# Kernel tuning notes

Hardware: AMD Instinct MI355X
Metric: run time of the kernel (lower is better)

Reference implementation:

```python
import jax, jax.numpy as jnp
import numpy as np

N = 20000   # nodes
E = 256000  # edges
G = 64      # graphs
EPS = 1e-5  # batchnorm eps


def setup_inputs() -> dict:
    key = jax.random.key(0)
    ks = jax.random.split(key, 20)
    inp = {}
    inp['x'] = jax.random.normal(ks[0], (N, 6), dtype=jnp.float32)
    inp['edge_index'] = jax.random.randint(ks[1], (2, E), 0, N)
    inp['batch'] = jnp.sort(jax.random.randint(ks[2], (N,), 0, G))
    conv_dims = [(6, 32), (32, 64), (64, 128), (128, 1024)]
    ki = 3
    for li, (a, b) in enumerate(conv_dims, 1):
        inp[f'W{li}'] = jax.random.normal(ks[ki], (a, b), dtype=jnp.float32) / np.sqrt(a).astype(np.float32); ki += 1
        inp[f'b{li}'] = jnp.zeros((b,), jnp.float32)
        inp[f'g{li}'] = jnp.ones((b,), jnp.float32)
        inp[f'be{li}'] = jnp.zeros((b,), jnp.float32)
    fc_dims = [(1024, 512), (512, 256), (256, 64)]
    for li, (a, b) in enumerate(fc_dims, 5):
        inp[f'W{li}'] = jax.random.normal(ks[ki], (a, b), dtype=jnp.float32) / np.sqrt(a).astype(np.float32); ki += 1
        inp[f'b{li}'] = jnp.zeros((b,), jnp.float32)
        if li < 7:
            inp[f'g{li}'] = jnp.ones((b,), jnp.float32)
            inp[f'be{li}'] = jnp.zeros((b,), jnp.float32)
    return inp


def _bn(h, g, be):
    # training-mode BatchNorm1d: biased variance over dim 0
    m = h.mean(axis=0)
    v = h.var(axis=0)
    return g * (h - m) * jax.lax.rsqrt(v + EPS) + be


def reference(x, edge_index, batch,
              W1, b1, g1, be1, W2, b2, g2, be2,
              W3, b3, g3, be3, W4, b4, g4, be4,
              W5, b5, g5, be5, W6, b6, g6, be6,
              W7, b7):
    loops = jnp.arange(N)
    src = jnp.concatenate([edge_index[0], loops])  # [E+N], message sources
    dst = jnp.concatenate([edge_index[1], loops])  # [E+N], aggregation targets
    deg = jax.ops.segment_sum(jnp.ones(E + N, x.dtype), dst, num_segments=N)
    dinv = jax.lax.rsqrt(deg)                      # deg >= 1 (self-loops)
    norm = dinv[src] * dinv[dst]                   # symmetric GCN normalization

    def gcn(h, W, b):
        h = h @ W                                   # [N, out]
        agg = jax.ops.segment_sum(norm[:, None] * h[src], dst, num_segments=N)
        return agg + b

    h = jax.nn.relu(_bn(gcn(x, W1, b1), g1, be1))
    h = jax.nn.relu(_bn(gcn(h, W2, b2), g2, be2))
    h = jax.nn.relu(_bn(gcn(h, W3, b3), g3, be3))
    h = jax.nn.relu(_bn(gcn(h, W4, b4), g4, be4))
    p = jax.ops.segment_max(h, batch, num_segments=G)  # global max pool [G, 1024]
    p = jax.nn.relu(_bn(p @ W5 + b5, g5, be5))
    p = jax.nn.relu(_bn(p @ W6 + b6, g6, be6))
    y = p @ W7 + b7
    n = jnp.maximum(jnp.linalg.norm(y, axis=1, keepdims=True), 1e-12)
    return y / n
```

## Files before the change

### kernel.cpp

```cpp
#include <hip/hip_runtime.h>
#include <math.h>

#define NN 20000
#define EE 256000
#define GG 64
#define CDIV(a,b) (((a)+(b)-1)/(b))
#define RB4 157

typedef __attribute__((ext_vector_type(8))) short bf16x8;
typedef __attribute__((ext_vector_type(4))) float f32x4;

__device__ __forceinline__ unsigned fkey(float f) {
  unsigned u = __float_as_uint(f);
  return (u & 0x80000000u) ? ~u : (u | 0x80000000u);
}
__device__ __forceinline__ float fdec(unsigned k) {
  unsigned u = (k & 0x80000000u) ? (k ^ 0x80000000u) : ~k;
  return __uint_as_float(u);
}
__device__ __forceinline__ unsigned short rne_bf16(float f) {
  unsigned u = __float_as_uint(f);
  unsigned r = (u + 0x7fffu + ((u >> 16) & 1u)) >> 16;
  return (unsigned short)r;
}


__global__ void k_prep(int* deg) {
  int i = blockIdx.x*blockDim.x + threadIdx.x;
  if (i < NN) deg[i] = 1;
}

__global__ void k_deg(const int* __restrict__ dst, int* deg) {
  int i = blockIdx.x*blockDim.x + threadIdx.x;
  if (i < EE) atomicAdd(&deg[dst[i]], 1);
}

__global__ __launch_bounds__(256) void k_scan_bsum(const int* __restrict__ deg,
                                                   int* __restrict__ bsum) {
  __shared__ int red[256];
  int b = blockIdx.x, t = threadIdx.x;
  int idx = b*1024 + t*4;
  int4 v = make_int4(0,0,0,0);
  if (idx < NN) v = *(const int4*)&deg[idx];
  red[t] = v.x + v.y + v.z + v.w;
  __syncthreads();
  for (int off = 128; off > 0; off >>= 1) {
    if (t < off) red[t] += red[t+off];
    __syncthreads();
  }
  if (t == 0) bsum[b] = red[0];
}

__global__ __launch_bounds__(256) void k_scan_apply(
    const int* __restrict__ deg, const int* __restrict__ bsum,
    int* __restrict__ offsets, int* __restrict__ cursor, float* __restrict__ dinv) {
  __shared__ int base_s;
  __shared__ int tsum[256];
  int b = blockIdx.x, t = threadIdx.x;
  if (t == 0) {
    int s = 0;
    for (int i = 0; i < b; ++i) s += bsum[i];
    base_s = s;
  }
  int idx = b*1024 + t*4;
  int4 v = make_int4(0,0,0,0);
  if (idx < NN) v = *(const int4*)&deg[idx];
  tsum[t] = v.x + v.y + v.z + v.w;
  __syncthreads();
  for (int off = 1; off < 256; off <<= 1) {
    int u = (t >= off) ? tsum[t-off] : 0;
    __syncthreads();
    tsum[t] += u;
    __syncthreads();
  }
  int excl = (t == 0) ? 0 : tsum[t-1];
  if (idx < NN) {
    int base = base_s + excl;
    int o0 = base;
    int o1 = o0 + v.x;
    int o2 = o1 + v.y;
    int o3 = o2 + v.z;
    *(int4*)&offsets[idx] = make_int4(o0,o1,o2,o3);
    *(int4*)&cursor[idx]  = make_int4(o0,o1,o2,o3);
    float4 dv;
    dv.x = rsqrtf((float)v.x); dv.y = rsqrtf((float)v.y);
    dv.z = rsqrtf((float)v.z); dv.w = rsqrtf((float)v.w);
    *(float4*)&dinv[idx] = dv;
    if (idx + 4 == NN) offsets[NN] = o3 + v.w;
  }
}

__global__ void k_fill(const int* __restrict__ srcv, const int* __restrict__ dstv,
                       const float* __restrict__ dinv, int* cursor,
                       int* __restrict__ csr_src, float* __restrict__ csr_w) {
  int i = blockIdx.x*blockDim.x + threadIdx.x;
  if (i < EE) {
    int s = srcv[i], d = dstv[i];
    int pos = atomicAdd(&cursor[d], 1);
    csr_src[pos] = s;
    csr_w[pos] = dinv[s] * dinv[d];
  } else if (i < EE + NN) {
    int n = i - EE;
    int pos = atomicAdd(&cursor[n], 1);
    csr_src[pos] = n;
    float di = dinv[n];
    csr_w[pos] = di * di;
  }
}


template<int C, int TX, int TY>
__global__ void k_agg(const float* __restrict__ in, const int* __restrict__ offsets,
                      const int* __restrict__ csr_src, const float* __restrict__ csr_w,
                      float* __restrict__ out) {
  int node = blockIdx.x * TY + threadIdx.y;
  if (node >= NN) return;
  int x = threadIdx.x;
  int k0 = offsets[node], k1 = offsets[node+1];
  if (x < C) {
    float acc = 0.f;
    for (int k = k0; k < k1; ++k) {
      int s = csr_src[k];
      float w = csr_w[k];
      acc += w * in[s*C + x];
    }
    out[node*C + x] = acc;
  }
}

template<int C, int TY>
__global__ void k_agg_f4(const float* __restrict__ in, const float* __restrict__ st,
                         const float* __restrict__ g, const float* __restrict__ be,
                         const int* __restrict__ offsets, const int* __restrict__ csr_src,
                         const float* __restrict__ csr_w, float* __restrict__ out) {
  int node = blockIdx.x*TY + threadIdx.y;
  if (node >= NN) return;
  int c0 = threadIdx.x*4;
  float4 mean = *(const float4*)&st[c0];
  float4 rstd = *(const float4*)&st[C+c0];
  float4 gv = *(const float4*)&g[c0];
  float4 bv = *(const float4*)&be[c0];
  float sx = gv.x*rstd.x, hx = bv.x - mean.x*sx;
  float sy = gv.y*rstd.y, hy = bv.y - mean.y*sy;
  float sz = gv.z*rstd.z, hz = bv.z - mean.z*sz;
  float sw = gv.w*rstd.w, hw = bv.w - mean.w*sw;
  int k0 = offsets[node], k1 = offsets[node+1];
  float a0=0.f,a1=0.f,a2=0.f,a3=0.f;
  for (int k = k0; k < k1; ++k) {
    int s = csr_src[k]; float w = csr_w[k];
    float4 v = *(const float4*)&in[s*C + c0];
    a0 += w*fmaxf(v.x*sx+hx, 0.f);
    a1 += w*fmaxf(v.y*sy+hy, 0.f);
    a2 += w*fmaxf(v.z*sz+hz, 0.f);
    a3 += w*fmaxf(v.w*sw+hw, 0.f);
  }
  *(float4*)&out[node*C+c0] = make_float4(a0,a1,a2,a3);
}

__global__ void k_agg_bf_f4(const float* __restrict__ in, const float* __restrict__ st,
                            const float* __restrict__ g, const float* __restrict__ be,
                            const int* __restrict__ offsets, const int* __restrict__ csr_src,
                            const float* __restrict__ csr_w, unsigned short* __restrict__ out) {
  int node = blockIdx.x*8 + threadIdx.y;
  if (node >= NN) return;
  int c0 = threadIdx.x*4;
  float4 mean = *(const float4*)&st[c0];
  float4 rstd = *(const float4*)&st[128+c0];
  float4 gv = *(const float4*)&g[c0];
  float4 bv = *(const float4*)&be[c0];
  float sx = gv.x*rstd.x, hx = bv.x - mean.x*sx;
  float sy = gv.y*rstd.y, hy = bv.y - mean.y*sy;
  float sz = gv.z*rstd.z, hz = bv.z - mean.z*sz;
  float sw = gv.w*rstd.w, hw = bv.w - mean.w*sw;
  int k0 = offsets[node], k1 = offsets[node+1];
  float a0=0.f,a1=0.f,a2=0.f,a3=0.f;
  for (int k = k0; k < k1; ++k) {
    int s = csr_src[k]; float w = csr_w[k];
    float4 v = *(const float4*)&in[s*128 + c0];
    a0 += w*fmaxf(v.x*sx+hx, 0.f);
    a1 += w*fmaxf(v.y*sy+hy, 0.f);
    a2 += w*fmaxf(v.z*sz+hz, 0.f);
    a3 += w*fmaxf(v.w*sw+hw, 0.f);
  }
  ushort4 o;
  o.x = rne_bf16(a0); o.y = rne_bf16(a1); o.z = rne_bf16(a2); o.w = rne_bf16(a3);
  *(ushort4*)&out[node*128 + c0] = o;
}

__global__ void k_wprep(const float* __restrict__ W, unsigned short* __restrict__ out) {
  int i = blockIdx.x*256 + threadIdx.x;
  if (i >= 128*1024) return;
  int k = i >> 10, c = i & 1023;
  out[c*128 + k] = rne_bf16(W[i]);
}


template<int K, int OUT, int ROWS>
__global__ __launch_bounds__(256) void k_gemm_small(
    const float* __restrict__ A, const float* __restrict__ W,
    float* __restrict__ out, float* __restrict__ pstats) {
  constexpr int RG  = 256 / OUT;
  constexpr int RPT = ROWS / RG;
  __shared__ float Ws[K*OUT];
  __shared__ float As[ROWS*K];
  __shared__ float reds[2][RG][OUT];
  int t = threadIdx.x;
  for (int i = t; i < K*OUT; i += 256) Ws[i] = W[i];
  int row0 = blockIdx.x * ROWS;
  for (int i = t; i < ROWS*K; i += 256) As[i] = A[row0*K + i];
  __syncthreads();
  int j  = t % OUT;
  int rg = t / OUT;
  float acc[RPT] = {};
  for (int k = 0; k < K; ++k) {
    float w = Ws[k*OUT + j];
    #pragma unroll
    for (int i = 0; i < RPT; ++i)
      acc[i] += As[(rg*RPT + i)*K + k] * w;
  }
  float s = 0.f, ss = 0.f;
  #pragma unroll
  for (int i = 0; i < RPT; ++i) {
    out[(row0 + rg*RPT + i)*OUT + j] = acc[i];
    s += acc[i]; ss += acc[i]*acc[i];
  }
  reds[0][rg][j] = s; reds[1][rg][j] = ss;
  __syncthreads();
  if (rg == 0) {
    float S = 0.f, SS = 0.f;
    #pragma unroll
    for (int r = 0; r < RG; ++r) { S += reds[0][r][j]; SS += reds[1][r][j]; }
    int p = blockIdx.x & 15;
    atomicAdd(&pstats[p*2*OUT + j], S);
    atomicAdd(&pstats[p*2*OUT + OUT + j], SS);
  }
}

template<int C>
__global__ void k_finalize_ps(const float* __restrict__ pstats, float* __restrict__ stats) {
  int c = blockIdx.x*64 + threadIdx.x;
  if (c >= C) return;
  float s = 0.f, ss = 0.f;
  #pragma unroll
  for (int p = 0; p < 16; ++p) { s += pstats[p*2*C + c]; ss += pstats[p*2*C + C + c]; }
  float m = s * (1.f/NN);
  float v = ss * (1.f/NN) - m*m;
  stats[c] = m;
  stats[C+c] = rsqrtf(v + 1e-5f);
}


__global__ __launch_bounds__(256) void k_gemm_l4_mfma(
    const unsigned short* __restrict__ A, const unsigned short* __restrict__ Bt,
    const int* __restrict__ batch,
    float* __restrict__ ps4, unsigned* __restrict__ pmax, unsigned* __restrict__ pmin) {
  __shared__ unsigned short As[128*128];
  __shared__ unsigned short Bs[128*128];
  int t = threadIdx.x;
  int row0 = blockIdx.x * 128;
  int col0 = blockIdx.y * 128;
  #pragma unroll
  for (int j = 0; j < 8; ++j) {
    int c = j*256 + t;
    int r = c >> 4, ck = c & 15;
    int rg = row0 + r;
    ulonglong2 v; v.x = 0; v.y = 0;
    if (rg < NN) v = *(const ulonglong2*)&A[rg*128 + ck*8];
    *(ulonglong2*)&As[r*128 + (ck ^ (r & 7))*8] = v;
  }
  #pragma unroll
  for (int j = 0; j < 8; ++j) {
    int c = j*256 + t;
    int r = c >> 4, ck = c & 15;
    ulonglong2 v = *(const ulonglong2*)&Bt[(col0 + r)*128 + ck*8];
    *(ulonglong2*)&Bs[r*128 + (ck ^ (r & 7))*8] = v;
  }
  __syncthreads();

  int w = t >> 6, l = t & 63;
  int wr = w >> 1, wc = w & 1;
  int lrow = l & 15, lk = l >> 4;
  f32x4 acc[4][4] = {};
  #pragma unroll
  for (int ks = 0; ks < 4; ++ks) {
    int kc = ks*4 + lk;
    bf16x8 a[4], b[4];
    #pragma unroll
    for (int m = 0; m < 4; ++m) {
      int r = wr*64 + m*16 + lrow;
      a[m] = *(const bf16x8*)&As[r*128 + (kc ^ (r & 7))*8];
    }
    #pragma unroll
    for (int n = 0; n < 4; ++n) {
      int r = wc*64 + n*16 + lrow;
      b[n] = *(const bf16x8*)&Bs[r*128 + (kc ^ (r & 7))*8];
    }
    #pragma unroll
    for (int m = 0; m < 4; ++m)
      #pragma unroll
      for (int n = 0; n < 4; ++n)
        acc[m][n] = __builtin_amdgcn_mfma_f32_16x16x32_bf16(a[m], b[n], acc[m][n], 0, 0, 0);
  }

  int rbase = row0 + wr*64;
  float s[4] = {}, ss[4] = {};
  float mx[4], mn[4];
  #pragma unroll
  for (int n = 0; n < 4; ++n) { mx[n] = -3.4e38f; mn[n] = 3.4e38f; }
  #pragma unroll
  for (int m = 0; m < 4; ++m)
    #pragma unroll
    for (int r = 0; r < 4; ++r) {
      int row_g = rbase + m*16 + lk*4 + r;
      if (row_g < NN) {
        #pragma unroll
        for (int n = 0; n < 4; ++n) {
          float v = acc[m][n][r];
          s[n] += v; ss[n] += v*v;
          mx[n] = fmaxf(mx[n], v); mn[n] = fminf(mn[n], v);
        }
      }
    }
  #pragma unroll
  for (int n = 0; n < 4; ++n) {
    s[n]  += __shfl_xor(s[n], 16);  s[n]  += __shfl_xor(s[n], 32);
    ss[n] += __shfl_xor(ss[n], 16); ss[n] += __shfl_xor(ss[n], 32);
  }

  int rlast_b = min(row0 + 127, NN - 1);
  int glo_b = batch[row0], ghi_b = batch[rlast_b];
  bool block_same = (glo_b == ghi_b);
  if (block_same) {
    #pragma unroll
    for (int n = 0; n < 4; ++n) {
      mx[n] = fmaxf(mx[n], __shfl_xor(mx[n], 16)); mx[n] = fmaxf(mx[n], __shfl_xor(mx[n], 32));
      mn[n] = fminf(mn[n], __shfl_xor(mn[n], 16)); mn[n] = fminf(mn[n], __shfl_xor(mn[n], 32));
    }
  }

  __syncthreads();
  float* scr_s = (float*)As;
  float* scr_p = (float*)Bs;
  if (l < 16) {
    #pragma unroll
    for (int n = 0; n < 4; ++n) {
      int si = (((wr*2 + wc)*4 + n)*16 + l)*2;
      scr_s[si]   = s[n];
      scr_s[si+1] = ss[n];
      if (block_same) { scr_p[si] = mx[n]; scr_p[si+1] = mn[n]; }
    }
  }
  __syncthreads();
  if (wr == 0 && l < 16) {
    #pragma unroll
    for (int n = 0; n < 4; ++n) {
      int si0 = (((0*2 + wc)*4 + n)*16 + l)*2;
      int si1 = (((1*2 + wc)*4 + n)*16 + l)*2;
      int cg  = col0 + wc*64 + n*16 + l;
      ps4[(size_t)blockIdx.x*2048 + cg]        = scr_s[si0]   + scr_s[si1];
      ps4[(size_t)blockIdx.x*2048 + 1024 + cg] = scr_s[si0+1] + scr_s[si1+1];
      if (block_same) {
        float bmx = fmaxf(scr_p[si0],   scr_p[si1]);
        float bmn = fminf(scr_p[si0+1], scr_p[si1+1]);
        if (bmx > -3.0e38f) atomicMax(&pmax[glo_b*1024 + cg], fkey(bmx));
        if (bmn <  3.0e38f) atomicMin(&pmin[glo_b*1024 + cg], fkey(bmn));
      }
    }
  }
  if (!block_same && rbase < NN) {
    int rlast = min(rbase + 63, NN - 1);
    int glo = batch[rbase], ghi = batch[rlast];
    if (glo == ghi) {
      #pragma unroll
      for (int n = 0; n < 4; ++n) {
        mx[n] = fmaxf(mx[n], __shfl_xor(mx[n], 16)); mx[n] = fmaxf(mx[n], __shfl_xor(mx[n], 32));
        mn[n] = fminf(mn[n], __shfl_xor(mn[n], 16)); mn[n] = fminf(mn[n], __shfl_xor(mn[n], 32));
      }
      if (l < 16) {
        #pragma unroll
        for (int n = 0; n < 4; ++n) {
          int cg = col0 + wc*64 + n*16 + l;
          atomicMax(&pmax[glo*1024 + cg], fkey(mx[n]));
          atomicMin(&pmin[glo*1024 + cg], fkey(mn[n]));
        }
      }
    } else {
      int gb[4][4];
      #pragma unroll
      for (int m = 0; m < 4; ++m)
        #pragma unroll
        for (int r = 0; r < 4; ++r) {
          int row_g = rbase + m*16 + lk*4 + r;
          gb[m][r] = (row_g < NN) ? batch[row_g] : -1;
        }
      for (int g = glo; g <= ghi; ++g) {
        float gmx[4], gmn[4];
        #pragma unroll
        for (int n = 0; n < 4; ++n) { gmx[n] = -3.4e38f; gmn[n] = 3.4e38f; }
        #pragma unroll
        for (int m = 0; m < 4; ++m)
          #pragma unroll
          for (int r = 0; r < 4; ++r) {
            bool in_g = (gb[m][r] == g);
            #pragma unroll
            for (int n = 0; n < 4; ++n) {
              float v = acc[m][n][r];
              gmx[n] = in_g ? fmaxf(gmx[n], v) : gmx[n];
              gmn[n] = in_g ? fminf(gmn[n], v) : gmn[n];
            }
          }
        #pragma unroll
        for (int n = 0; n < 4; ++n) {
          gmx[n] = fmaxf(gmx[n], __shfl_xor(gmx[n], 16)); gmx[n] = fmaxf(gmx[n], __shfl_xor(gmx[n], 32));
          gmn[n] = fminf(gmn[n], __shfl_xor(gmn[n], 16)); gmn[n] = fminf(gmn[n], __shfl_xor(gmn[n], 32));
        }
        if (l < 16) {
          #pragma unroll
          for (int n = 0; n < 4; ++n) {
            int cg = col0 + wc*64 + n*16 + l;
            if (gmx[n] > -3.0e38f) atomicMax(&pmax[g*1024 + cg], fkey(gmx[n]));
            if (gmn[n] <  3.0e38f) atomicMin(&pmin[g*1024 + cg], fkey(gmn[n]));
          }
        }
      }
    }
  }
}

__global__ void k_finalize_l4(const float* __restrict__ ps4, float* __restrict__ stats) {
  int c = blockIdx.x*256 + threadIdx.x;
  float s = 0.f, ss = 0.f;
  #pragma unroll 8
  for (int rb = 0; rb < RB4; ++rb) {
    s  += ps4[(size_t)rb*2048 + c];
    ss += ps4[(size_t)rb*2048 + 1024 + c];
  }
  float m = s * (1.f/NN);
  float v = ss * (1.f/NN) - m*m;
  stats[c] = m;
  stats[1024 + c] = rsqrtf(v + 1e-5f);
}

__global__ void k_bnpool(const unsigned* __restrict__ pmax, const unsigned* __restrict__ pmin,
                         const float* __restrict__ stats, const float* __restrict__ g,
                         const float* __restrict__ be, float* __restrict__ p) {
  int i = blockIdx.x*256 + threadIdx.x;
  if (i >= 64*1024) return;
  int c = i & 1023;
  float mean = stats[c], rstd = stats[1024+c];
  float sc = g[c]*rstd, sh = be[c] - mean*sc;
  float v = (sc >= 0.f) ? fdec(pmax[i]) : fdec(pmin[i]);
  p[i] = fmaxf(v*sc + sh, 0.f);
}


template<int K, int OUT, int KT>
__global__ __launch_bounds__(256) void k_fc_tile(
    const float* __restrict__ A, const float* __restrict__ W,
    float* __restrict__ out) {
  __shared__ float As[64][KT];
  __shared__ float Ws[KT][64];
  int t = threadIdx.y*64 + threadIdx.x;
  int j0 = blockIdx.x*64;
  int k0 = blockIdx.y*KT;
  #pragma unroll 4
  for (int i = t; i < 64*KT/4; i += 256) {
    int r  = i / (KT/4);
    int c4 = i % (KT/4);
    float4 v = *(const float4*)&A[r*K + k0 + c4*4];
    *(float4*)&As[r][c4*4] = v;
  }
  #pragma unroll 4
  for (int i = t; i < KT*16; i += 256) {
    int k  = i / 16;
    int c4 = i % 16;
    float4 v = *(const float4*)&W[(k0+k)*OUT + j0 + c4*4];
    *(float4*)&Ws[k][c4*4] = v;
  }
  __syncthreads();
  int j  = threadIdx.x;
  int r0 = threadIdx.y*16;
  float acc[16] = {};
  for (int kk = 0; kk < KT; ++kk) {
    float w = Ws[kk][j];
    #pragma unroll
    for (int i = 0; i < 16; ++i) acc[i] += As[r0+i][kk] * w;
  }
  #pragma unroll
  for (int i = 0; i < 16; ++i) atomicAdd(&out[(r0+i)*OUT + j0 + j], acc[i]);
}

__global__ __launch_bounds__(512) void k_bn_rows(
    float* __restrict__ h, const float* __restrict__ g,
    const float* __restrict__ be, int C) {
  int c = blockIdx.x*64 + threadIdx.x;
  int y = threadIdx.y;
  float v[8];
  float s = 0.f, ss = 0.f;
  #pragma unroll
  for (int i = 0; i < 8; ++i) {
    v[i] = h[(y*8+i)*C + c];
    s += v[i]; ss += v[i]*v[i];
  }
  __shared__ float rs[8][64], rss[8][64], bc[2][64];
  rs[y][threadIdx.x] = s; rss[y][threadIdx.x] = ss;
  __syncthreads();
  if (y == 0) {
    s = 0.f; ss = 0.f;
    #pragma unroll
    for (int i = 0; i < 8; ++i) { s += rs[i][threadIdx.x]; ss += rss[i][threadIdx.x]; }
    float m = s*(1.f/64.f);
    float var = ss*(1.f/64.f) - m*m;
    float rstd = rsqrtf(var + 1e-5f);
    float sc = g[c]*rstd;
    bc[0][threadIdx.x] = sc;
    bc[1][threadIdx.x] = be[c] - m*sc;
  }
  __syncthreads();
  float sc = bc[0][threadIdx.x], sh = bc[1][threadIdx.x];
  #pragma unroll
  for (int i = 0; i < 8; ++i)
    h[(y*8+i)*C + c] = fmaxf(v[i]*sc + sh, 0.f);
}

__global__ void k_l2norm(const float* __restrict__ in, const float* __restrict__ b,
                         float* __restrict__ out) {
  int r = blockIdx.x, j = threadIdx.x;
  float v = in[r*64 + j] + b[j];
  float ss = v*v;
  #pragma unroll
  for (int off = 1; off < 64; off <<= 1) ss += __shfl_xor(ss, off);
  float inv = 1.f / fmaxf(sqrtf(ss), 1e-12f);
  out[r*64 + j] = v * inv;
}


extern "C" void kernel_launch(void* const* d_in, const int* in_sizes, int n_in,
                              void* d_out, int out_size, void* d_ws, size_t ws_size,
                              hipStream_t stream) {
  const float* x    = (const float*)d_in[0];
  const int*   ei   = (const int*)d_in[1];
  const int*   batch= (const int*)d_in[2];
  const float* W1=(const float*)d_in[3],  *g1=(const float*)d_in[5],  *be1=(const float*)d_in[6];
  const float* W2=(const float*)d_in[7],  *g2=(const float*)d_in[9],  *be2=(const float*)d_in[10];
  const float* W3=(const float*)d_in[11], *g3=(const float*)d_in[13], *be3=(const float*)d_in[14];
  const float* W4=(const float*)d_in[15], *g4=(const float*)d_in[17], *be4=(const float*)d_in[18];
  const float* W5=(const float*)d_in[19], *g5=(const float*)d_in[21], *be5=(const float*)d_in[22];
  const float* W6=(const float*)d_in[23], *g6=(const float*)d_in[25], *be6=(const float*)d_in[26];
  const float* W7=(const float*)d_in[27], *b7=(const float*)d_in[28];
  const int* esrc = ei;
  const int* edst = ei + EE;

  char* w = (char*)d_ws;
  auto alloc = [&](size_t bytes) -> void* {
    void* p = (void*)w;
    w += (bytes + 255) & ~(size_t)255;
    return p;
  };
  int*   deg     = (int*)  alloc(NN*4);
  int*   offsets = (int*)  alloc((NN+1)*4);
  int*   cursor  = (int*)  alloc(NN*4);
  int*   bsum    = (int*)  alloc(32*4);
  float* dinv    = (float*)alloc(NN*4);
  int*   csr_src = (int*)  alloc((EE+NN)*4);
  float* csr_w   = (float*)alloc((EE+NN)*4);
  float* stats1  = (float*)alloc(2*32*4);
  float* stats2  = (float*)alloc(2*64*4);
  float* stats3  = (float*)alloc(2*128*4);
  float* stats4  = (float*)alloc(2*1024*4);
  float* pstats  = (float*)alloc(16*2*128*4);
  float* ps4     = (float*)alloc((size_t)RB4*2048*4);
  float* agg     = (float*)alloc((size_t)NN*128*4);
  float* hbufA   = (float*)alloc((size_t)NN*128*4);
  float* hbufB   = (float*)alloc((size_t)NN*64*4);
  float* pooled  = (float*)alloc(64*1024*4);
  float* fc1     = (float*)alloc(64*512*4);
  float* fc2     = (float*)alloc(64*256*4);
  float* fc3raw  = (float*)alloc(64*64*4);
  unsigned short* agg_bf = (unsigned short*)alloc((size_t)NN*128*2);
  unsigned short* wt_bf  = (unsigned short*)alloc(1024*128*2);
  unsigned* pmax = (unsigned*)alloc(64*1024*4);
  unsigned* pmin = (unsigned*)alloc(64*1024*4);

  k_prep<<<CDIV(NN,256),256,0,stream>>>(deg);
  k_deg<<<CDIV(EE,256),256,0,stream>>>(edst, deg);
  k_scan_bsum<<<20,256,0,stream>>>(deg, bsum);
  k_scan_apply<<<20,256,0,stream>>>(deg, bsum, offsets, cursor, dinv);
  k_fill<<<CDIV(EE+NN,256),256,0,stream>>>(esrc, edst, dinv, cursor, csr_src, csr_w);

  k_agg<6,8,32><<<CDIV(NN,32),dim3(8,32),0,stream>>>(x, offsets, csr_src, csr_w, agg);
  hipMemsetAsync(pstats, 0, 16*2*32*4, stream);
  k_gemm_small<6,32,32><<<NN/32,256,0,stream>>>(agg, W1, hbufA, pstats);
  k_finalize_ps<32><<<1,64,0,stream>>>(pstats, stats1);

  k_agg_f4<32,32><<<CDIV(NN,32),dim3(8,32),0,stream>>>(hbufA, stats1, g1, be1, offsets, csr_src, csr_w, agg);
  hipMemsetAsync(pstats, 0, 16*2*64*4, stream);
  k_gemm_small<32,64,16><<<NN/16,256,0,stream>>>(agg, W2, hbufB, pstats);
  k_finalize_ps<64><<<1,64,0,stream>>>(pstats, stats2);

  k_agg_f4<64,16><<<CDIV(NN,16),dim3(16,16),0,stream>>>(hbufB, stats2, g2, be2, offsets, csr_src, csr_w, agg);
  hipMemsetAsync(pstats, 0, 16*2*128*4, stream);
  k_gemm_small<64,128,16><<<NN/16,256,0,stream>>>(agg, W3, hbufA, pstats);
  k_finalize_ps<128><<<2,64,0,stream>>>(pstats, stats3);

  k_agg_bf_f4<<<CDIV(NN,8),dim3(32,8),0,stream>>>(hbufA, stats3, g3, be3, offsets, csr_src, csr_w, agg_bf);
  k_wprep<<<CDIV(128*1024,256),256,0,stream>>>(W4, wt_bf);
  hipMemsetAsync(pmax, 0x00, 64*1024*4, stream);
  hipMemsetAsync(pmin, 0xFF, 64*1024*4, stream);
  k_gemm_l4_mfma<<<dim3(RB4,8),256,0,stream>>>(agg_bf, wt_bf, batch, ps4, pmax, pmin);
  k_finalize_l4<<<4,256,0,stream>>>(ps4, stats4);
  k_bnpool<<<CDIV(64*1024,256),256,0,stream>>>(pmax, pmin, stats4, g4, be4, pooled);

  hipMemsetAsync(fc1, 0, 64*512*4, stream);
  k_fc_tile<1024,512,128><<<dim3(8,8),dim3(64,4),0,stream>>>(pooled, W5, fc1);
  k_bn_rows<<<8,dim3(64,8),0,stream>>>(fc1, g5, be5, 512);

  hipMemsetAsync(fc2, 0, 64*256*4, stream);
  k_fc_tile<512,256,128><<<dim3(4,4),dim3(64,4),0,stream>>>(fc1, W6, fc2);
  k_bn_rows<<<4,dim3(64,8),0,stream>>>(fc2, g6, be6, 256);

  hipMemsetAsync(fc3raw, 0, 64*64*4, stream);
  k_fc_tile<256,64,64><<<dim3(1,4),dim3(64,4),0,stream>>>(fc2, W7, fc3raw);
  k_l2norm<<<64,64,0,stream>>>(fc3raw, b7, (float*)d_out);
}
```

Before: 357.4 us.

## Unroll aggregation edge loops by two and reuse A tile across two column tiles

The aggregation kernels now process two edges per iteration with separate accumulators, which raises memory-level parallelism on the gathered loads. The layer-4 MFMA GEMM now loops over two 128-column tiles per block while keeping the A tile resident in LDS. This halves the grid's y dimension and the number of A tile reloads. The reduction scratch moves into dedicated shared arrays, which adds LDS use and an extra barrier per column tile, and leaves fewer blocks in flight.

```diff
diff --git a/kernel.cpp b/kernel.cpp
--- a/kernel.cpp
+++ b/kernel.cpp
@@ -145,16 +145,32 @@
   float sz = gv.z*rstd.z, hz = bv.z - mean.z*sz;
   float sw = gv.w*rstd.w, hw = bv.w - mean.w*sw;
   int k0 = offsets[node], k1 = offsets[node+1];
-  float a0=0.f,a1=0.f,a2=0.f,a3=0.f;
-  for (int k = k0; k < k1; ++k) {
-    int s = csr_src[k]; float w = csr_w[k];
-    float4 v = *(const float4*)&in[s*C + c0];
-    a0 += w*fmaxf(v.x*sx+hx, 0.f);
-    a1 += w*fmaxf(v.y*sy+hy, 0.f);
-    a2 += w*fmaxf(v.z*sz+hz, 0.f);
-    a3 += w*fmaxf(v.w*sw+hw, 0.f);
-  }
-  *(float4*)&out[node*C+c0] = make_float4(a0,a1,a2,a3);
+  float p0=0.f,p1=0.f,p2=0.f,p3=0.f;
+  float q0=0.f,q1=0.f,q2=0.f,q3=0.f;
+  int k = k0;
+  for (; k + 2 <= k1; k += 2) {
+    int s0 = csr_src[k], s1 = csr_src[k+1];
+    float w0 = csr_w[k], w1 = csr_w[k+1];
+    float4 u = *(const float4*)&in[s0*C + c0];
+    float4 v = *(const float4*)&in[s1*C + c0];
+    p0 += w0*fmaxf(u.x*sx+hx, 0.f);
+    p1 += w0*fmaxf(u.y*sy+hy, 0.f);
+    p2 += w0*fmaxf(u.z*sz+hz, 0.f);
+    p3 += w0*fmaxf(u.w*sw+hw, 0.f);
+    q0 += w1*fmaxf(v.x*sx+hx, 0.f);
+    q1 += w1*fmaxf(v.y*sy+hy, 0.f);
+    q2 += w1*fmaxf(v.z*sz+hz, 0.f);
+    q3 += w1*fmaxf(v.w*sw+hw, 0.f);
+  }
+  if (k < k1) {
+    int s0 = csr_src[k]; float w0 = csr_w[k];
+    float4 u = *(const float4*)&in[s0*C + c0];
+    p0 += w0*fmaxf(u.x*sx+hx, 0.f);
+    p1 += w0*fmaxf(u.y*sy+hy, 0.f);
+    p2 += w0*fmaxf(u.z*sz+hz, 0.f);
+    p3 += w0*fmaxf(u.w*sw+hw, 0.f);
+  }
+  *(float4*)&out[node*C+c0] = make_float4(p0+q0, p1+q1, p2+q2, p3+q3);
 }
 
 __global__ void k_agg_bf_f4(const float* __restrict__ in, const float* __restrict__ st,
@@ -173,17 +189,34 @@
   float sz = gv.z*rstd.z, hz = bv.z - mean.z*sz;
   float sw = gv.w*rstd.w, hw = bv.w - mean.w*sw;
   int k0 = offsets[node], k1 = offsets[node+1];
-  float a0=0.f,a1=0.f,a2=0.f,a3=0.f;
-  for (int k = k0; k < k1; ++k) {
-    int s = csr_src[k]; float w = csr_w[k];
-    float4 v = *(const float4*)&in[s*128 + c0];
-    a0 += w*fmaxf(v.x*sx+hx, 0.f);
-    a1 += w*fmaxf(v.y*sy+hy, 0.f);
-    a2 += w*fmaxf(v.z*sz+hz, 0.f);
-    a3 += w*fmaxf(v.w*sw+hw, 0.f);
+  float p0=0.f,p1=0.f,p2=0.f,p3=0.f;
+  float q0=0.f,q1=0.f,q2=0.f,q3=0.f;
+  int k = k0;
+  for (; k + 2 <= k1; k += 2) {
+    int s0 = csr_src[k], s1 = csr_src[k+1];
+    float w0 = csr_w[k], w1 = csr_w[k+1];
+    float4 u = *(const float4*)&in[s0*128 + c0];
+    float4 v = *(const float4*)&in[s1*128 + c0];
+    p0 += w0*fmaxf(u.x*sx+hx, 0.f);
+    p1 += w0*fmaxf(u.y*sy+hy, 0.f);
+    p2 += w0*fmaxf(u.z*sz+hz, 0.f);
+    p3 += w0*fmaxf(u.w*sw+hw, 0.f);
+    q0 += w1*fmaxf(v.x*sx+hx, 0.f);
+    q1 += w1*fmaxf(v.y*sy+hy, 0.f);
+    q2 += w1*fmaxf(v.z*sz+hz, 0.f);
+    q3 += w1*fmaxf(v.w*sw+hw, 0.f);
+  }
+  if (k < k1) {
+    int s0 = csr_src[k]; float w0 = csr_w[k];
+    float4 u = *(const float4*)&in[s0*128 + c0];
+    p0 += w0*fmaxf(u.x*sx+hx, 0.f);
+    p1 += w0*fmaxf(u.y*sy+hy, 0.f);
+    p2 += w0*fmaxf(u.z*sz+hz, 0.f);
+    p3 += w0*fmaxf(u.w*sw+hw, 0.f);
   }
   ushort4 o;
-  o.x = rne_bf16(a0); o.y = rne_bf16(a1); o.z = rne_bf16(a2); o.w = rne_bf16(a3);
+  o.x = rne_bf16(p0+q0); o.y = rne_bf16(p1+q1);
+  o.z = rne_bf16(p2+q2); o.w = rne_bf16(p3+q3);
   *(ushort4*)&out[node*128 + c0] = o;
 }
 
@@ -256,170 +289,171 @@
     float* __restrict__ ps4, unsigned* __restrict__ pmax, unsigned* __restrict__ pmin) {
   __shared__ unsigned short As[128*128];
   __shared__ unsigned short Bs[128*128];
+  __shared__ float scr_s[512];
+  __shared__ float scr_p[512];
   int t = threadIdx.x;
   int row0 = blockIdx.x * 128;
-  int col0 = blockIdx.y * 128;
   #pragma unroll
   for (int j = 0; j < 8; ++j) {
     int c = j*256 + t;
     int r = c >> 4, ck = c & 15;
     int rg = row0 + r;
     ulonglong2 v; v.x = 0; v.y = 0;
-    if (rg < NN) v = *(const ulonglong2*)&A[rg*128 + ck*8];
+    if (rg < NN) v = *(const ulonglong2*)&A[(size_t)rg*128 + ck*8];
     *(ulonglong2*)&As[r*128 + (ck ^ (r & 7))*8] = v;
   }
-  #pragma unroll
-  for (int j = 0; j < 8; ++j) {
-    int c = j*256 + t;
-    int r = c >> 4, ck = c & 15;
-    ulonglong2 v = *(const ulonglong2*)&Bt[(col0 + r)*128 + ck*8];
-    *(ulonglong2*)&Bs[r*128 + (ck ^ (r & 7))*8] = v;
-  }
-  __syncthreads();
-
   int w = t >> 6, l = t & 63;
   int wr = w >> 1, wc = w & 1;
   int lrow = l & 15, lk = l >> 4;
-  f32x4 acc[4][4] = {};
-  #pragma unroll
-  for (int ks = 0; ks < 4; ++ks) {
-    int kc = ks*4 + lk;
-    bf16x8 a[4], b[4];
-    #pragma unroll
-    for (int m = 0; m < 4; ++m) {
-      int r = wr*64 + m*16 + lrow;
-      a[m] = *(const bf16x8*)&As[r*128 + (kc ^ (r & 7))*8];
-    }
-    #pragma unroll
-    for (int n = 0; n < 4; ++n) {
-      int r = wc*64 + n*16 + lrow;
-      b[n] = *(const bf16x8*)&Bs[r*128 + (kc ^ (r & 7))*8];
-    }
-    #pragma unroll
-    for (int m = 0; m < 4; ++m)
-      #pragma unroll
-      for (int n = 0; n < 4; ++n)
-        acc[m][n] = __builtin_amdgcn_mfma_f32_16x16x32_bf16(a[m], b[n], acc[m][n], 0, 0, 0);
-  }
-
   int rbase = row0 + wr*64;
-  float s[4] = {}, ss[4] = {};
-  float mx[4], mn[4];
-  #pragma unroll
-  for (int n = 0; n < 4; ++n) { mx[n] = -3.4e38f; mn[n] = 3.4e38f; }
-  #pragma unroll
-  for (int m = 0; m < 4; ++m)
-    #pragma unroll
-    for (int r = 0; r < 4; ++r) {
-      int row_g = rbase + m*16 + lk*4 + r;
-      if (row_g < NN) {
-        #pragma unroll
-        for (int n = 0; n < 4; ++n) {
-          float v = acc[m][n][r];
-          s[n] += v; ss[n] += v*v;
-          mx[n] = fmaxf(mx[n], v); mn[n] = fminf(mn[n], v);
-        }
-      }
-    }
-  #pragma unroll
-  for (int n = 0; n < 4; ++n) {
-    s[n]  += __shfl_xor(s[n], 16);  s[n]  += __shfl_xor(s[n], 32);
-    ss[n] += __shfl_xor(ss[n], 16); ss[n] += __shfl_xor(ss[n], 32);
-  }
-
   int rlast_b = min(row0 + 127, NN - 1);
   int glo_b = batch[row0], ghi_b = batch[rlast_b];
   bool block_same = (glo_b == ghi_b);
-  if (block_same) {
+
+  for (int p = 0; p < 2; ++p) {
+    int col0 = (blockIdx.y*2 + p)*128;
+    if (p) __syncthreads();
+    #pragma unroll
+    for (int j = 0; j < 8; ++j) {
+      int c = j*256 + t;
+      int r = c >> 4, ck = c & 15;
+      ulonglong2 v = *(const ulonglong2*)&Bt[(size_t)(col0 + r)*128 + ck*8];
+      *(ulonglong2*)&Bs[r*128 + (ck ^ (r & 7))*8] = v;
+    }
+    __syncthreads();
+
+    f32x4 acc[4][4] = {};
+    #pragma unroll
+    for (int ks = 0; ks < 4; ++ks) {
+      int kc = ks*4 + lk;
+      bf16x8 a[4], b[4];
+      #pragma unroll
+      for (int m = 0; m < 4; ++m) {
+        int r = wr*64 + m*16 + lrow;
+        a[m] = *(const bf16x8*)&As[r*128 + (kc ^ (r & 7))*8];
+      }
+      #pragma unroll
+      for (int n = 0; n < 4; ++n) {
+        int r = wc*64 + n*16 + lrow;
+        b[n] = *(const bf16x8*)&Bs[r*128 + (kc ^ (r & 7))*8];
+      }
+      #pragma unroll
+      for (int m = 0; m < 4; ++m)
+        #pragma unroll
+        for (int n = 0; n < 4; ++n)
+          acc[m][n] = __builtin_amdgcn_mfma_f32_16x16x32_bf16(a[m], b[n], acc[m][n], 0, 0, 0);
+    }
+
+    float s[4] = {}, ss[4] = {};
+    float mx[4], mn[4];
+    #pragma unroll
+    for (int n = 0; n < 4; ++n) { mx[n] = -3.4e38f; mn[n] = 3.4e38f; }
+    #pragma unroll
+    for (int m = 0; m < 4; ++m)
+      #pragma unroll
+      for (int r = 0; r < 4; ++r) {
+        int row_g = rbase + m*16 + lk*4 + r;
+        if (row_g < NN) {
+          #pragma unroll
+          for (int n = 0; n < 4; ++n) {
+            float v = acc[m][n][r];
+            s[n] += v; ss[n] += v*v;
+            mx[n] = fmaxf(mx[n], v); mn[n] = fminf(mn[n], v);
+          }
+        }
+      }
     #pragma unroll
     for (int n = 0; n < 4; ++n) {
-      mx[n] = fmaxf(mx[n], __shfl_xor(mx[n], 16)); mx[n] = fmaxf(mx[n], __shfl_xor(mx[n], 32));
-      mn[n] = fminf(mn[n], __shfl_xor(mn[n], 16)); mn[n] = fminf(mn[n], __shfl_xor(mn[n], 32));
-    }
-  }
-
-  __syncthreads();
-  float* scr_s = (float*)As;
-  float* scr_p = (float*)Bs;
-  if (l < 16) {
-    #pragma unroll
-    for (int n = 0; n < 4; ++n) {
-      int si = (((wr*2 + wc)*4 + n)*16 + l)*2;
-      scr_s[si]   = s[n];
-      scr_s[si+1] = ss[n];
-      if (block_same) { scr_p[si] = mx[n]; scr_p[si+1] = mn[n]; }
-    }
-  }
-  __syncthreads();
-  if (wr == 0 && l < 16) {
-    #pragma unroll
-    for (int n = 0; n < 4; ++n) {
-      int si0 = (((0*2 + wc)*4 + n)*16 + l)*2;
-      int si1 = (((1*2 + wc)*4 + n)*16 + l)*2;
-      int cg  = col0 + wc*64 + n*16 + l;
-      ps4[(size_t)blockIdx.x*2048 + cg]        = scr_s[si0]   + scr_s[si1];
-      ps4[(size_t)blockIdx.x*2048 + 1024 + cg] = scr_s[si0+1] + scr_s[si1+1];
-      if (block_same) {
-        float bmx = fmaxf(scr_p[si0],   scr_p[si1]);
-        float bmn = fminf(scr_p[si0+1], scr_p[si1+1]);
-        if (bmx > -3.0e38f) atomicMax(&pmax[glo_b*1024 + cg], fkey(bmx));
-        if (bmn <  3.0e38f) atomicMin(&pmin[glo_b*1024 + cg], fkey(bmn));
-      }
-    }
-  }
-  if (!block_same && rbase < NN) {
-    int rlast = min(rbase + 63, NN - 1);
-    int glo = batch[rbase], ghi = batch[rlast];
-    if (glo == ghi) {
+      s[n]  += __shfl_xor(s[n], 16);  s[n]  += __shfl_xor(s[n], 32);
+      ss[n] += __shfl_xor(ss[n], 16); ss[n] += __shfl_xor(ss[n], 32);
+    }
+    if (block_same) {
       #pragma unroll
       for (int n = 0; n < 4; ++n) {
         mx[n] = fmaxf(mx[n], __shfl_xor(mx[n], 16)); mx[n] = fmaxf(mx[n], __shfl_xor(mx[n], 32));
         mn[n] = fminf(mn[n], __shfl_xor(mn[n], 16)); mn[n] = fminf(mn[n], __shfl_xor(mn[n], 32));
       }
-      if (l < 16) {
+    }
+    if (l < 16) {
+      #pragma unroll
+      for (int n = 0; n < 4; ++n) {
+        int si = (((wr*2 + wc)*4 + n)*16 + l)*2;
+        scr_s[si]   = s[n];
+        scr_s[si+1] = ss[n];
+        if (block_same) { scr_p[si] = mx[n]; scr_p[si+1] = mn[n]; }
+      }
+    }
+    __syncthreads();
+    if (wr == 0 && l < 16) {
+      #pragma unroll
+      for (int n = 0; n < 4; ++n) {
+        int si0 = (((0*2 + wc)*4 + n)*16 + l)*2;
+        int si1 = (((1*2 + wc)*4 + n)*16 + l)*2;
+        int cg  = col0 + wc*64 + n*16 + l;
+        ps4[(size_t)blockIdx.x*2048 + cg]        = scr_s[si0]   + scr_s[si1];
+        ps4[(size_t)blockIdx.x*2048 + 1024 + cg] = scr_s[si0+1] + scr_s[si1+1];
+        if (block_same) {
+          float bmx = fmaxf(scr_p[si0],   scr_p[si1]);
+          float bmn = fminf(scr_p[si0+1], scr_p[si1+1]);
+          if (bmx > -3.0e38f) atomicMax(&pmax[glo_b*1024 + cg], fkey(bmx));
+          if (bmn <  3.0e38f) atomicMin(&pmin[glo_b*1024 + cg], fkey(bmn));
+        }
+      }
+    }
+    if (!block_same && rbase < NN) {
+      int rlast = min(rbase + 63, NN - 1);
+      int glo = batch[rbase], ghi = batch[rlast];
+      if (glo == ghi) {
         #pragma unroll
         for (int n = 0; n < 4; ++n) {
-          int cg = col0 + wc*64 + n*16 + l;
-          atomicMax(&pmax[glo*1024 + cg], fkey(mx[n]));
-          atomicMin(&pmin[glo*1024 + cg], fkey(mn[n]));
-        }
-      }
-    } else {
-      int gb[4][4];
-      #pragma unroll
-      for (int m = 0; m < 4; ++m)
-        #pragma unroll
-        for (int r = 0; r < 4; ++r) {
-          int row_g = rbase + m*16 + lk*4 + r;
-          gb[m][r] = (row_g < NN) ? batch[row_g] : -1;
-        }
-      for (int g = glo; g <= ghi; ++g) {
-        float gmx[4], gmn[4];
-        #pragma unroll
-        for (int n = 0; n < 4; ++n) { gmx[n] = -3.4e38f; gmn[n] = 3.4e38f; }
-        #pragma unroll
-        for (int m = 0; m < 4; ++m)
-          #pragma unroll
-          for (int r = 0; r < 4; ++r) {
-            bool in_g = (gb[m][r] == g);
-            #pragma unroll
-            for (int n = 0; n < 4; ++n) {
-              float v = acc[m][n][r];
-              gmx[n] = in_g ? fmaxf(gmx[n], v) : gmx[n];
-              gmn[n] = in_g ? fminf(gmn[n], v) : gmn[n];
-            }
-          }
-        #pragma unroll
-        for (int n = 0; n < 4; ++n) {
-          gmx[n] = fmaxf(gmx[n], __shfl_xor(gmx[n], 16)); gmx[n] = fmaxf(gmx[n], __shfl_xor(gmx[n], 32));
-          gmn[n] = fminf(gmn[n], __shfl_xor(gmn[n], 16)); gmn[n] = fminf(gmn[n], __shfl_xor(gmn[n], 32));
+          mx[n] = fmaxf(mx[n], __shfl_xor(mx[n], 16)); mx[n] = fmaxf(mx[n], __shfl_xor(mx[n], 32));
+          mn[n] = fminf(mn[n], __shfl_xor(mn[n], 16)); mn[n] = fminf(mn[n], __shfl_xor(mn[n], 32));
         }
         if (l < 16) {
           #pragma unroll
           for (int n = 0; n < 4; ++n) {
             int cg = col0 + wc*64 + n*16 + l;
-            if (gmx[n] > -3.0e38f) atomicMax(&pmax[g*1024 + cg], fkey(gmx[n]));
-            if (gmn[n] <  3.0e38f) atomicMin(&pmin[g*1024 + cg], fkey(gmn[n]));
+            atomicMax(&pmax[glo*1024 + cg], fkey(mx[n]));
+            atomicMin(&pmin[glo*1024 + cg], fkey(mn[n]));
+          }
+        }
+      } else {
+        int gb[4][4];
+        #pragma unroll
+        for (int m = 0; m < 4; ++m)
+          #pragma unroll
+          for (int r = 0; r < 4; ++r) {
+            int row_g = rbase + m*16 + lk*4 + r;
+            gb[m][r] = (row_g < NN) ? batch[row_g] : -1;
+          }
+        for (int g = glo; g <= ghi; ++g) {
+          float gmx[4], gmn[4];
+          #pragma unroll
+          for (int n = 0; n < 4; ++n) { gmx[n] = -3.4e38f; gmn[n] = 3.4e38f; }
+          #pragma unroll
+          for (int m = 0; m < 4; ++m)
+            #pragma unroll
+            for (int r = 0; r < 4; ++r) {
+              bool in_g = (gb[m][r] == g);
+              #pragma unroll
+              for (int n = 0; n < 4; ++n) {
+                float v = acc[m][n][r];
+                gmx[n] = in_g ? fmaxf(gmx[n], v) : gmx[n];
+                gmn[n] = in_g ? fminf(gmn[n], v) : gmn[n];
+              }
+            }
+          #pragma unroll
+          for (int n = 0; n < 4; ++n) {
+            gmx[n] = fmaxf(gmx[n], __shfl_xor(gmx[n], 16)); gmx[n] = fmaxf(gmx[n], __shfl_xor(gmx[n], 32));
+            gmn[n] = fminf(gmn[n], __shfl_xor(gmn[n], 16)); gmn[n] = fminf(gmn[n], __shfl_xor(gmn[n], 32));
+          }
+          if (l < 16) {
+            #pragma unroll
+            for (int n = 0; n < 4; ++n) {
+              int cg = col0 + wc*64 + n*16 + l;
+              if (gmx[n] > -3.0e38f) atomicMax(&pmax[g*1024 + cg], fkey(gmx[n]));
+              if (gmn[n] <  3.0e38f) atomicMin(&pmin[g*1024 + cg], fkey(gmn[n]));
+            }
           }
         }
       }
@@ -607,7 +641,7 @@
   k_wprep<<<CDIV(128*1024,256),256,0,stream>>>(W4, wt_bf);
   hipMemsetAsync(pmax, 0x00, 64*1024*4, stream);
   hipMemsetAsync(pmin, 0xFF, 64*1024*4, stream);
-  k_gemm_l4_mfma<<<dim3(RB4,8),256,0,stream>>>(agg_bf, wt_bf, batch, ps4, pmax, pmin);
+  k_gemm_l4_mfma<<<dim3(RB4,4),256,0,stream>>>(agg_bf, wt_bf, batch, ps4, pmax, pmin);
   k_finalize_l4<<<4,256,0,stream>>>(ps4, stats4);
   k_bnpool<<<CDIV(64*1024,256),256,0,stream>>>(pmax, pmin, stats4, g4, be4, pooled);
 
```

New measurement: 337.3 us. 5.6% less time.
